# Kernel tuning notes

Measured on AMD Instinct MI355X. Metric: run time of the kernel, lower is better.

The kernel has to match this reference:

```python
import jax, jax.numpy as jnp
import numpy as np

N, F, H, B = 8192, 128, 64, 8


def setup_inputs() -> dict:
    key = jax.random.key(0)
    ks = jax.random.split(key, 8)
    x = jax.random.normal(ks[0], (N, F), jnp.float32)
    pos = jax.random.normal(ks[1], (N, 3), jnp.float32)
    batch = jnp.sort(jax.random.randint(ks[2], (N,), 0, B)).astype(jnp.int64)
    cell = jax.random.normal(ks[3], (B, 3, 3), jnp.float32)
    # charge-head MLP params (Linear(F,H) -> SiLU -> Linear(H,1))
    W1 = jax.random.normal(ks[4], (F, H), jnp.float32) * (1.0 / np.sqrt(F))
    b1 = jnp.zeros((H,), jnp.float32)
    W2 = jax.random.normal(ks[5], (H, 1), jnp.float32) * (1.0 / np.sqrt(H))
    b2 = jnp.zeros((1,), jnp.float32)
    screening = jnp.float32(0.2)   # screening_init
    softening = jnp.float32(0.5)   # softening_init
    return {"x": x, "pos": pos, "cell": cell, "W1": W1, "b1": b1,
            "W2": W2, "b2": b2, "screening": screening,
            "softening": softening, "batch": batch}


def reference(x, pos, cell, W1, b1, W2, b2, screening, softening, batch):
    n_graphs = cell.shape[0]
    n = pos.shape[0]
    # latent scalar charge per atom
    h = jax.nn.silu(x @ W1 + b1)                       # [N,H]
    q = (h @ W2 + b2)[:, 0]                            # [N]
    # neutralize: subtract per-graph mean charge
    counts = jnp.clip(jax.ops.segment_sum(jnp.ones_like(q), batch,
                                          num_segments=n_graphs), 1.0)
    mean_q = jax.ops.segment_sum(q, batch, num_segments=n_graphs) / counts
    q = q - mean_q[batch]
    # dense all-pairs screened Coulomb (nonperiodic)
    delta = pos[None, :, :] - pos[:, None, :]          # [N,N,3]
    r = jnp.sqrt(jnp.sum(delta * delta, axis=-1) + softening * softening)
    kern = jnp.exp(-screening * r) / r                 # [N,N]
    same_graph = batch[None, :] == batch[:, None]
    idx = jnp.arange(n)
    mask = same_graph & (idx[None, :] != idx[:, None])
    kern = jnp.where(mask, kern, 0.0)
    pair_energy = 0.5 * (q[:, None] * q[None, :]) * kern
    atom_energy = jnp.sum(pair_energy, axis=1, keepdims=True)  # [N,1]
    return atom_energy
```

## Files before the change

kernel.cpp:

```cpp
#include <hip/hip_runtime.h>
#include <math.h>

#define NATOMS 8192
#define NF 128
#define NH 64
#define NB 8

#define TI 32
#define TJ 256
#define JS 8

#define OFF_BATCH32 0
#define OFF_Q       32768
#define OFF_GSUM    65536
#define OFF_GSTART  65600

__global__ __launch_bounds__(256) void fused1_kernel(
    const float* __restrict__ x, const float* __restrict__ W1,
    const float* __restrict__ b1, const float* __restrict__ W2,
    const float* __restrict__ b2, const void* __restrict__ batch_raw,
    int* __restrict__ batch32, int* __restrict__ gstart,
    float* __restrict__ q) {
    const int* v32 = (const int*)batch_raw;
    const long long* v64 = (const long long*)batch_raw;
    const int tid = threadIdx.x;

    if (blockIdx.x == 2048) {
        const bool is64 = (v32[NATOMS - 1] == 0);
        if (tid <= NB) {
            if (tid == NB) {
                gstart[NB] = NATOMS;
            } else {
                int lo = 0, hi = NATOMS;
                while (lo < hi) {
                    int mid = (lo + hi) >> 1;
                    int v = is64 ? (int)v64[mid] : v32[mid];
                    if (v < tid) lo = mid + 1; else hi = mid;
                }
                gstart[tid] = lo;
            }
        }
        return;
    }

    const int gt = blockIdx.x * 256 + tid;
    if (gt < NATOMS) {
        const bool is64 = (v32[NATOMS - 1] == 0);
        batch32[gt] = is64 ? (int)v64[gt] : v32[gt];
    }

    const int atom = gt >> 6;
    const int lane = tid & 63;

    const float* xr = x + atom * NF;
    float z = b1[lane];
#pragma unroll
    for (int f0 = 0; f0 < NF; f0 += 4) {
        const float4 xv = *(const float4*)(xr + f0);
        z = fmaf(xv.x, W1[(f0 + 0) * NH + lane], z);
        z = fmaf(xv.y, W1[(f0 + 1) * NH + lane], z);
        z = fmaf(xv.z, W1[(f0 + 2) * NH + lane], z);
        z = fmaf(xv.w, W1[(f0 + 3) * NH + lane], z);
    }
    const float h = z / (1.0f + __expf(-z));
    float t = h * W2[lane];
#pragma unroll
    for (int m = 32; m >= 1; m >>= 1) t += __shfl_xor(t, m, 64);
    if (lane == 0) q[atom] = t + b2[0];
}

__global__ __launch_bounds__(256) void gsum_kernel(
    const float* __restrict__ q, const int* __restrict__ gstart,
    float* __restrict__ gsum) {
    __shared__ float part[4];
    const int g = blockIdx.x;
    const int s = gstart[g], e = gstart[g + 1];
    float t = 0.0f;
    for (int i = s + threadIdx.x; i < e; i += 256) t += q[i];
#pragma unroll
    for (int m = 32; m >= 1; m >>= 1) t += __shfl_xor(t, m, 64);
    if ((threadIdx.x & 63) == 0) part[threadIdx.x >> 6] = t;
    __syncthreads();
    if (threadIdx.x == 0) gsum[g] = part[0] + part[1] + part[2] + part[3];
}

__global__ __launch_bounds__(256) void pairfin_kernel(
    const float* __restrict__ pos, const float* __restrict__ q,
    const int* __restrict__ batch32, const int* __restrict__ gstart,
    const float* __restrict__ gsum, float* __restrict__ out,
    const float* __restrict__ scr_p, const float* __restrict__ soft_p) {
    __shared__ float4 tile[TJ];
    __shared__ float smean[NB];
    __shared__ float psum[JS * TI];

    const int tid = threadIdx.x;
    const int ii = tid & (TI - 1);
    const int js = tid >> 5;

    if (tid < NB) {
        const int c = gstart[tid + 1] - gstart[tid];
        smean[tid] = gsum[tid] / (float)(c > 0 ? c : 1);
    }
    __syncthreads();

    const float scr = *scr_p;
    const float soft = *soft_p;
    const float soft2 = soft * soft;

    const int i0 = blockIdx.x * TI;
    const int i = i0 + ii;
    const int gi = batch32[i];
    const int si = gstart[gi];
    const unsigned span = (unsigned)(gstart[gi + 1] - si);
    const float pix = pos[3 * i + 0];
    const float piy = pos[3 * i + 1];
    const float piz = pos[3 * i + 2];

    const int jlo = gstart[batch32[i0]];
    const int jhi = gstart[batch32[i0 + TI - 1] + 1];

    float acc = 0.0f;
    for (int jt = jlo; jt < jhi; jt += TJ) {
        __syncthreads();
        const int jj = jt + tid;
        float4 v;
        if (jj < jhi) {
            v.x = pos[3 * jj + 0];
            v.y = pos[3 * jj + 1];
            v.z = pos[3 * jj + 2];
            v.w = q[jj] - smean[batch32[jj]];
        } else {
            v.x = v.y = v.z = v.w = 0.0f;
        }
        tile[tid] = v;
        __syncthreads();

        const int cnt = min(TJ, jhi - jt);
        const int ue = min(js * 32 + 32, cnt);
        for (int u = js * 32; u < ue; ++u) {
            const float4 p = tile[u];
            const float dx = p.x - pix;
            const float dy = p.y - piy;
            const float dz = p.z - piz;
            float d2 = fmaf(dx, dx, soft2);
            d2 = fmaf(dy, dy, d2);
            d2 = fmaf(dz, dz, d2);
            const float rinv = rsqrtf(d2);
            const float r = d2 * rinv;
            const float e = __expf(-scr * r);
            const int j = jt + u;
            const float w = ((unsigned)(j - si) < span) ? p.w : 0.0f;
            acc = fmaf(w * e, rinv, acc);
        }
    }
    psum[js * TI + ii] = acc;
    __syncthreads();

    if (tid < TI) {
        float tot = 0.0f;
#pragma unroll
        for (int k = 0; k < JS; ++k) tot += psum[k * TI + tid];
        const float mean = smean[gi];
        const float qn = q[i] - mean;
        const float sa = fabsf(soft);
        const float selfk = __expf(-scr * sa) / sa;
        out[i] = 0.5f * qn * (tot - qn * selfk);
    }
}

extern "C" void kernel_launch(void* const* d_in, const int* in_sizes, int n_in,
                              void* d_out, int out_size, void* d_ws, size_t ws_size,
                              hipStream_t stream) {
    const float* x    = (const float*)d_in[0];
    const float* pos  = (const float*)d_in[1];
    const float* W1   = (const float*)d_in[3];
    const float* b1   = (const float*)d_in[4];
    const float* W2   = (const float*)d_in[5];
    const float* b2   = (const float*)d_in[6];
    const float* scr  = (const float*)d_in[7];
    const float* soft = (const float*)d_in[8];
    const void*  braw = (const void*)d_in[9];

    char* ws = (char*)d_ws;
    int*   batch32 = (int*)(ws + OFF_BATCH32);
    float* q       = (float*)(ws + OFF_Q);
    float* gsum    = (float*)(ws + OFF_GSUM);
    int*   gstart  = (int*)(ws + OFF_GSTART);
    float* out     = (float*)d_out;

    fused1_kernel<<<2049, 256, 0, stream>>>(x, W1, b1, W2, b2, braw,
                                            batch32, gstart, q);
    gsum_kernel<<<NB, 256, 0, stream>>>(q, gstart, gsum);
    pairfin_kernel<<<NATOMS / TI, 256, 0, stream>>>(pos, q, batch32, gstart,
                                                    gsum, out, scr, soft);
}
```

Before: 120.1 us.

## Fuse per-graph mean into pair kernel, halve atom tile, split MLP accumulators

```diff
diff --git a/kernel.cpp b/kernel.cpp
--- a/kernel.cpp
+++ b/kernel.cpp
@@ -6,14 +6,13 @@
 #define NH 64
 #define NB 8
 
-#define TI 32
+#define TI 16
 #define TJ 256
-#define JS 8
+#define JS 16
 
 #define OFF_BATCH32 0
 #define OFF_Q       32768
-#define OFF_GSUM    65536
-#define OFF_GSTART  65600
+#define OFF_GSTART  65536
 
 __global__ __launch_bounds__(256) void fused1_kernel(
     const float* __restrict__ x, const float* __restrict__ W1,
@@ -53,15 +52,21 @@
     const int lane = tid & 63;
 
     const float* xr = x + atom * NF;
-    float z = b1[lane];
+    float z0 = b1[lane], z1 = 0.0f;
 #pragma unroll
-    for (int f0 = 0; f0 < NF; f0 += 4) {
-        const float4 xv = *(const float4*)(xr + f0);
-        z = fmaf(xv.x, W1[(f0 + 0) * NH + lane], z);
-        z = fmaf(xv.y, W1[(f0 + 1) * NH + lane], z);
-        z = fmaf(xv.z, W1[(f0 + 2) * NH + lane], z);
-        z = fmaf(xv.w, W1[(f0 + 3) * NH + lane], z);
+    for (int f0 = 0; f0 < NF; f0 += 8) {
+        const float4 xa = *(const float4*)(xr + f0);
+        const float4 xb = *(const float4*)(xr + f0 + 4);
+        z0 = fmaf(xa.x, W1[(f0 + 0) * NH + lane], z0);
+        z1 = fmaf(xa.y, W1[(f0 + 1) * NH + lane], z1);
+        z0 = fmaf(xa.z, W1[(f0 + 2) * NH + lane], z0);
+        z1 = fmaf(xa.w, W1[(f0 + 3) * NH + lane], z1);
+        z0 = fmaf(xb.x, W1[(f0 + 4) * NH + lane], z0);
+        z1 = fmaf(xb.y, W1[(f0 + 5) * NH + lane], z1);
+        z0 = fmaf(xb.z, W1[(f0 + 6) * NH + lane], z0);
+        z1 = fmaf(xb.w, W1[(f0 + 7) * NH + lane], z1);
     }
+    const float z = z0 + z1;
     const float h = z / (1.0f + __expf(-z));
     float t = h * W2[lane];
 #pragma unroll
@@ -69,45 +74,44 @@
     if (lane == 0) q[atom] = t + b2[0];
 }
 
-__global__ __launch_bounds__(256) void gsum_kernel(
-    const float* __restrict__ q, const int* __restrict__ gstart,
-    float* __restrict__ gsum) {
-    __shared__ float part[4];
-    const int g = blockIdx.x;
-    const int s = gstart[g], e = gstart[g + 1];
-    float t = 0.0f;
-    for (int i = s + threadIdx.x; i < e; i += 256) t += q[i];
-#pragma unroll
-    for (int m = 32; m >= 1; m >>= 1) t += __shfl_xor(t, m, 64);
-    if ((threadIdx.x & 63) == 0) part[threadIdx.x >> 6] = t;
-    __syncthreads();
-    if (threadIdx.x == 0) gsum[g] = part[0] + part[1] + part[2] + part[3];
-}
-
 __global__ __launch_bounds__(256) void pairfin_kernel(
     const float* __restrict__ pos, const float* __restrict__ q,
     const int* __restrict__ batch32, const int* __restrict__ gstart,
-    const float* __restrict__ gsum, float* __restrict__ out,
+    float* __restrict__ out,
     const float* __restrict__ scr_p, const float* __restrict__ soft_p) {
     __shared__ float4 tile[TJ];
     __shared__ float smean[NB];
+    __shared__ float red[4];
     __shared__ float psum[JS * TI];
 
     const int tid = threadIdx.x;
     const int ii = tid & (TI - 1);
-    const int js = tid >> 5;
+    const int js = tid >> 4;
 
-    if (tid < NB) {
-        const int c = gstart[tid + 1] - gstart[tid];
-        smean[tid] = gsum[tid] / (float)(c > 0 ? c : 1);
+    const int i0 = blockIdx.x * TI;
+    const int gfirst = batch32[i0];
+    const int glast = batch32[i0 + TI - 1];
+
+    for (int g = gfirst; g <= glast; ++g) {
+        const int s = gstart[g], e = gstart[g + 1];
+        float t = 0.0f;
+        for (int idx = s + tid; idx < e; idx += 256) t += q[idx];
+#pragma unroll
+        for (int m = 32; m >= 1; m >>= 1) t += __shfl_xor(t, m, 64);
+        if ((tid & 63) == 0) red[tid >> 6] = t;
+        __syncthreads();
+        if (tid == 0) {
+            const int c = e - s;
+            smean[g] = (red[0] + red[1] + red[2] + red[3]) /
+                       (float)(c > 0 ? c : 1);
+        }
+        __syncthreads();
     }
-    __syncthreads();
 
     const float scr = *scr_p;
     const float soft = *soft_p;
     const float soft2 = soft * soft;
 
-    const int i0 = blockIdx.x * TI;
     const int i = i0 + ii;
     const int gi = batch32[i];
     const int si = gstart[gi];
@@ -116,8 +120,8 @@
     const float piy = pos[3 * i + 1];
     const float piz = pos[3 * i + 2];
 
-    const int jlo = gstart[batch32[i0]];
-    const int jhi = gstart[batch32[i0 + TI - 1] + 1];
+    const int jlo = gstart[gfirst];
+    const int jhi = gstart[glast + 1];
 
     float acc = 0.0f;
     for (int jt = jlo; jt < jhi; jt += TJ) {
@@ -136,8 +140,9 @@
         __syncthreads();
 
         const int cnt = min(TJ, jhi - jt);
-        const int ue = min(js * 32 + 32, cnt);
-        for (int u = js * 32; u < ue; ++u) {
+        const int base = jt - si;
+        const int ue = min(js * TI + TI, cnt);
+        for (int u = js * TI; u < ue; ++u) {
             const float4 p = tile[u];
             const float dx = p.x - pix;
             const float dy = p.y - piy;
@@ -148,8 +153,7 @@
             const float rinv = rsqrtf(d2);
             const float r = d2 * rinv;
             const float e = __expf(-scr * r);
-            const int j = jt + u;
-            const float w = ((unsigned)(j - si) < span) ? p.w : 0.0f;
+            const float w = ((unsigned)(base + u) < span) ? p.w : 0.0f;
             acc = fmaf(w * e, rinv, acc);
         }
     }
@@ -160,8 +164,7 @@
         float tot = 0.0f;
 #pragma unroll
         for (int k = 0; k < JS; ++k) tot += psum[k * TI + tid];
-        const float mean = smean[gi];
-        const float qn = q[i] - mean;
+        const float qn = q[i] - smean[gi];
         const float sa = fabsf(soft);
         const float selfk = __expf(-scr * sa) / sa;
         out[i] = 0.5f * qn * (tot - qn * selfk);
@@ -184,13 +187,11 @@
     char* ws = (char*)d_ws;
     int*   batch32 = (int*)(ws + OFF_BATCH32);
     float* q       = (float*)(ws + OFF_Q);
-    float* gsum    = (float*)(ws + OFF_GSUM);
     int*   gstart  = (int*)(ws + OFF_GSTART);
     float* out     = (float*)d_out;
 
     fused1_kernel<<<2049, 256, 0, stream>>>(x, W1, b1, W2, b2, braw,
                                             batch32, gstart, q);
-    gsum_kernel<<<NB, 256, 0, stream>>>(q, gstart, gsum);
     pairfin_kernel<<<NATOMS / TI, 256, 0, stream>>>(pos, q, batch32, gstart,
-                                                    gsum, out, scr, soft);
+                                                    out, scr, soft);
 }
```

New measurement: 106.4 us. 11.4% less time.
